# Kernel optimization log

Measured on AMD Instinct MI355X. Metric: run time of the kernel, lower is better.

The kernel has to match this reference:

```python
import jax, jax.numpy as jnp
import numpy as np

B, N_L, N_T, H, G = 8, 48, 512, 128, 10
BN_EPS = 1e-5


def setup_inputs() -> dict:
    key = jax.random.key(0)
    ks = jax.random.split(key, 16)
    inp = {
        "lig_s": jax.random.normal(ks[0], (B * N_L, H), dtype=jnp.float32),
        "lig_pos": jax.random.normal(ks[1], (B * N_L, 3), dtype=jnp.float32) * 5.0,
        "lig_batch": jnp.repeat(jnp.arange(B, dtype=jnp.int64), N_L),
        "pro_s": jax.random.normal(ks[2], (B * N_T, H), dtype=jnp.float32),
        "pro_pos": jax.random.normal(ks[3], (B * N_T, 3), dtype=jnp.float32) * 20.0,
        "pro_batch": jnp.repeat(jnp.arange(B, dtype=jnp.int64), N_T),
        # MLP: Linear(H,H) + BatchNorm1d(H) (eval mode) + ELU (+ Dropout off in eval)
        "W1": jax.random.normal(ks[4], (H, H), dtype=jnp.float32) / np.sqrt(H),
        "b1": jax.random.normal(ks[5], (H,), dtype=jnp.float32) * 0.01,
        "bn_gamma": 1.0 + 0.1 * jax.random.normal(ks[6], (H,), dtype=jnp.float32),
        "bn_beta": 0.1 * jax.random.normal(ks[7], (H,), dtype=jnp.float32),
        "bn_mean": 0.1 * jax.random.normal(ks[8], (H,), dtype=jnp.float32),
        "bn_var": 0.5 + jax.random.uniform(ks[9], (H,), dtype=jnp.float32),
        "W_pi": jax.random.normal(ks[10], (G, H), dtype=jnp.float32) / np.sqrt(H),
        "b_pi": jnp.zeros((G,), dtype=jnp.float32),
        "W_sigma": jax.random.normal(ks[11], (G, H), dtype=jnp.float32) / np.sqrt(H),
        "b_sigma": jnp.zeros((G,), dtype=jnp.float32),
        "W_mu": jax.random.normal(ks[12], (G, H), dtype=jnp.float32) / np.sqrt(H),
        "b_mu": jnp.zeros((G,), dtype=jnp.float32),
    }
    return inp


def _forward(lig_s, lig_pos, pro_s, pro_pos,
             W1, b1, bn_gamma, bn_beta, bn_mean, bn_var,
             W_pi, b_pi, W_sigma, b_sigma, W_mu, b_mu):
    # to_dense_batch with uniform graph sizes == reshape; C_mask is all-True,
    # so C[C_mask] == reshape(B*N_l*N_t, H).
    h_l = lig_s.reshape(B, N_L, H)
    h_t = pro_s.reshape(B, N_T, H)
    # broadcast pairwise sum: [B, N_l, N_t, H] -> compact to [M, H]
    C = (h_l[:, :, None, :] + h_t[:, None, :, :]).reshape(B * N_L * N_T, H)
    # MLP (eval mode): Linear -> BatchNorm1d(running stats) -> ELU
    C = C @ W1.T + b1
    C = (C - bn_mean) * jax.lax.rsqrt(bn_var + BN_EPS) * bn_gamma + bn_beta
    C = jax.nn.elu(C)
    pi = jax.nn.softmax(C @ W_pi.T + b_pi, axis=-1)
    sigma = jax.nn.elu(C @ W_sigma.T + b_sigma) + 1.1
    mu = jax.nn.elu(C @ W_mu.T + b_mu) + 1.0
    # pairwise Euclidean distances via -2*X@Y^T + |Y|^2 + |X|^2 (torch uses fp64;
    # fp32 here), then sqrt; compacted and detached.
    Xl = lig_pos.reshape(B, N_L, 3)
    Xt = pro_pos.reshape(B, N_T, 3)
    d2 = (-2.0 * jnp.einsum("bld,btd->blt", Xl, Xt)
          + jnp.sum(Xt * Xt, axis=-1)[:, None, :]
          + jnp.sum(Xl * Xl, axis=-1)[:, :, None])
    dist = jnp.sqrt(d2).reshape(B * N_L * N_T)
    dist = jax.lax.stop_gradient(dist[:, None])  # [M, 1]
    C_batch = jnp.repeat(jnp.arange(B, dtype=jnp.int64), N_L * N_T)
    return pi, sigma, mu, dist, C_batch


def reference(lig_s, lig_pos, lig_batch, pro_s, pro_pos, pro_batch,
              W1, b1, bn_gamma, bn_beta, bn_mean, bn_var,
              W_pi, b_pi, W_sigma, b_sigma, W_mu, b_mu):
    del lig_batch, pro_batch  # uniform segments -> reshape handles densification
    return _forward(lig_s, lig_pos, pro_s, pro_pos,
                    W1, b1, bn_gamma, bn_beta, bn_mean, bn_var,
                    W_pi, b_pi, W_sigma, b_sigma, W_mu, b_mu)
```

## Files before the change

### kernel.cpp

```cpp
#include <hip/hip_runtime.h>
#include <math.h>

constexpr int kB  = 8;
constexpr int kNL = 48;
constexpr int kNT = 512;
constexpr int kH  = 128;
constexpr int kG  = 10;

constexpr int kRowsL = kB * kNL;
constexpr int kRowsT = kB * kNT;
constexpr int kRows  = kRowsL + kRowsT;
constexpr int kM     = kB * kNL * kNT;
constexpr float kEps = 1e-5f;

constexpr size_t OFF_PI = 0;
constexpr size_t OFF_SG = (size_t)kM * kG;
constexpr size_t OFF_MU = 2 * (size_t)kM * kG;
constexpr size_t OFF_D  = 3 * (size_t)kM * kG;
constexpr size_t OFF_CB = OFF_D + kM;

typedef __attribute__((ext_vector_type(8))) short short8;
typedef __attribute__((ext_vector_type(4))) float f32x4;

__device__ __forceinline__ short f2bf(float f) {
    unsigned u = __builtin_bit_cast(unsigned, f);
    unsigned r = u + 0x7fffu + ((u >> 16) & 1u);
    return (short)(r >> 16);
}
__device__ __forceinline__ float elu_f(float x) {
    return x > 0.0f ? x : (__expf(x) - 1.0f);
}

__global__ __launch_bounds__(256) void pack_kernel(
    const float* __restrict__ W1, const float* __restrict__ b1,
    const float* __restrict__ gamma, const float* __restrict__ beta,
    const float* __restrict__ mean, const float* __restrict__ var,
    const float* __restrict__ Wpi, const float* __restrict__ Wsg,
    const float* __restrict__ Wmu,
    short* __restrict__ W1p, short* __restrict__ Wcp, float* __restrict__ bias_l)
{
    const int tid = threadIdx.x;
    __shared__ float s_s[kH];
    if (tid < kH) {
        float s = gamma[tid] * rsqrtf(var[tid] + kEps);
        s_s[tid] = s;
        bias_l[tid] = (b1[tid] - mean[tid]) * s + beta[tid];
    }
    __syncthreads();

    for (int idx = tid; idx < 4 * 8 * 64; idx += 256) {
        const int kt = idx >> 9, nt = (idx >> 6) & 7, lane = idx & 63;
        const int c  = nt * 16 + (lane & 15);
        const int k0 = kt * 32 + (lane >> 4) * 8;
        const float s = s_s[c];
        const float* wr = W1 + (size_t)c * kH + k0;
        short8 v;
#pragma unroll
        for (int j = 0; j < 8; ++j) v[j] = f2bf(wr[j] * s);
        *((short8*)W1p + idx) = v;
    }
    for (int idx = tid; idx < 4 * 3 * 64; idx += 256) {
        const int kt = idx / 192, rem = idx % 192, nt = rem >> 6, lane = rem & 63;
        const int n  = lane & 15;
        const int k0 = kt * 32 + (lane >> 4) * 8;
        const float* W = (nt == 0) ? Wpi : ((nt == 1) ? Wsg : Wmu);
        short8 v;
        if (n < kG) {
            const float* wr = W + (size_t)n * kH + k0;
#pragma unroll
            for (int j = 0; j < 8; ++j) v[j] = f2bf(wr[j]);
        } else {
#pragma unroll
            for (int j = 0; j < 8; ++j) v[j] = 0;
        }
        *((short8*)Wcp + idx) = v;
    }
}

__global__ __launch_bounds__(256) void prep_mfma(
    const float* __restrict__ lig_s, const float* __restrict__ pro_s,
    const short* __restrict__ W1p, const float* __restrict__ bias_l,
    float* __restrict__ Al, float* __restrict__ At)
{
    const int mtile = blockIdx.x;
    const int wave = threadIdx.x >> 6, lane = threadIdx.x & 63;
    const int q = lane >> 4, n16 = lane & 15;

    short8 bfrag[2][4];
    const short8* wp = (const short8*)W1p;
#pragma unroll
    for (int kt = 0; kt < 4; ++kt)
#pragma unroll
        for (int h = 0; h < 2; ++h)
            bfrag[h][kt] = wp[(kt * 8 + (2 * wave + h)) * 64 + lane];

    const int row = mtile * 16 + n16;
    const bool lig = (row < kRowsL);
    const float* X = lig ? (lig_s + (size_t)row * kH)
                         : (pro_s + (size_t)(row - kRowsL) * kH);

    f32x4 acc[2] = {};
#pragma unroll
    for (int kt = 0; kt < 4; ++kt) {
        const float4* xp = (const float4*)(X + kt * 32 + q * 8);
        float4 x0 = xp[0], x1 = xp[1];
        short8 a;
        a[0] = f2bf(x0.x); a[1] = f2bf(x0.y); a[2] = f2bf(x0.z); a[3] = f2bf(x0.w);
        a[4] = f2bf(x1.x); a[5] = f2bf(x1.y); a[6] = f2bf(x1.z); a[7] = f2bf(x1.w);
        acc[0] = __builtin_amdgcn_mfma_f32_16x16x32_bf16(a, bfrag[0][kt], acc[0], 0, 0, 0);
        acc[1] = __builtin_amdgcn_mfma_f32_16x16x32_bf16(a, bfrag[1][kt], acc[1], 0, 0, 0);
    }

#pragma unroll
    for (int h = 0; h < 2; ++h) {
        const int c = (2 * wave + h) * 16 + n16;
        const float bi = lig ? bias_l[c] : 0.0f;
#pragma unroll
        for (int r = 0; r < 4; ++r) {
            const int R = mtile * 16 + q * 4 + r;
            const float v = acc[h][r] + bi;
            if (lig) Al[(size_t)R * kH + c] = v;
            else     At[(size_t)(R - kRowsL) * kH + c] = v;
        }
    }
}

__global__ __launch_bounds__(256) void pair_mfma(
    const float* __restrict__ Al, const float* __restrict__ At,
    const short* __restrict__ Wcp,
    const float* __restrict__ bpi, const float* __restrict__ bsg,
    const float* __restrict__ bmu,
    float* __restrict__ out)
{
    const int blk = blockIdx.x;
    const int bl = blk >> 2, tch = blk & 3;
    const int wave = threadIdx.x >> 6, lane = threadIdx.x & 63;
    const int q = lane >> 4, n = lane & 15;
    const int b = bl / kNL;
    const int t0 = tch * 128 + wave * 32;

    short8 bf[3][4];
    const short8* wp = (const short8*)Wcp;
#pragma unroll
    for (int kt = 0; kt < 4; ++kt)
#pragma unroll
        for (int ntl = 0; ntl < 3; ++ntl)
            bf[ntl][kt] = wp[(kt * 3 + ntl) * 64 + lane];

    const int nc = (n < kG) ? n : (kG - 1);
    const float bias0 = (n < kG) ? bpi[nc] : 0.0f;
    const float bias1 = (n < kG) ? bsg[nc] : 0.0f;
    const float bias2 = (n < kG) ? bmu[nc] : 0.0f;

    const float* alp = Al + (size_t)bl * kH;
    f32x4 acc[2][3] = {};

#pragma unroll
    for (int mt = 0; mt < 2; ++mt) {
        const int t = t0 + mt * 16 + n;
        const float* atp = At + (size_t)(b * kNT + t) * kH;
#pragma unroll
        for (int kt = 0; kt < 4; ++kt) {
            const float4* ap4 = (const float4*)(alp + kt * 32 + q * 8);
            const float4* tp4 = (const float4*)(atp + kt * 32 + q * 8);
            float4 a0 = ap4[0], a1 = ap4[1];
            float4 t0v = tp4[0], t1v = tp4[1];
            short8 a;
            a[0] = f2bf(elu_f(a0.x + t0v.x)); a[1] = f2bf(elu_f(a0.y + t0v.y));
            a[2] = f2bf(elu_f(a0.z + t0v.z)); a[3] = f2bf(elu_f(a0.w + t0v.w));
            a[4] = f2bf(elu_f(a1.x + t1v.x)); a[5] = f2bf(elu_f(a1.y + t1v.y));
            a[6] = f2bf(elu_f(a1.z + t1v.z)); a[7] = f2bf(elu_f(a1.w + t1v.w));
            acc[mt][0] = __builtin_amdgcn_mfma_f32_16x16x32_bf16(a, bf[0][kt], acc[mt][0], 0, 0, 0);
            acc[mt][1] = __builtin_amdgcn_mfma_f32_16x16x32_bf16(a, bf[1][kt], acc[mt][1], 0, 0, 0);
            acc[mt][2] = __builtin_amdgcn_mfma_f32_16x16x32_bf16(a, bf[2][kt], acc[mt][2], 0, 0, 0);
        }
    }

    const int pairbase = bl * kNT + t0;
#pragma unroll
    for (int mt = 0; mt < 2; ++mt) {
#pragma unroll
        for (int r = 0; r < 4; ++r) {
            const float lg = acc[mt][0][r] + bias0;
            float mx = (n < kG) ? lg : -3.0e38f;
#pragma unroll
            for (int d = 1; d < 16; d <<= 1) mx = fmaxf(mx, __shfl_xor(mx, d));
            const float e = (n < kG) ? __expf(lg - mx) : 0.0f;
            float sm = e;
#pragma unroll
            for (int d = 1; d < 16; d <<= 1) sm += __shfl_xor(sm, d);
            const int m = pairbase + mt * 16 + q * 4 + r;
            if (n < kG) out[OFF_PI + (size_t)m * kG + n] = e / sm;
        }
#pragma unroll
        for (int r = 0; r < 4; ++r) {
            const int m = pairbase + mt * 16 + q * 4 + r;
            if (n < kG) {
                out[OFF_SG + (size_t)m * kG + n] = elu_f(acc[mt][1][r] + bias1) + 1.1f;
                out[OFF_MU + (size_t)m * kG + n] = elu_f(acc[mt][2][r] + bias2) + 1.0f;
            }
        }
    }
}

__global__ __launch_bounds__(256) void dist_kernel(
    const float* __restrict__ lig_pos, const float* __restrict__ pro_pos,
    float* __restrict__ out)
{
    const int idx = blockIdx.x * 256 + threadIdx.x;
    const int bl = idx >> 9, t = idx & 511;
    const int b = bl / kNL;
    const int pr = b * kNT + t;
    const float dx = lig_pos[(size_t)bl * 3 + 0] - pro_pos[(size_t)pr * 3 + 0];
    const float dy = lig_pos[(size_t)bl * 3 + 1] - pro_pos[(size_t)pr * 3 + 1];
    const float dz = lig_pos[(size_t)bl * 3 + 2] - pro_pos[(size_t)pr * 3 + 2];
    out[OFF_D + idx] = sqrtf(dx * dx + dy * dy + dz * dz);
    out[OFF_CB + idx] = (float)b;
}

extern "C" void kernel_launch(void* const* d_in, const int* in_sizes, int n_in,
                              void* d_out, int out_size, void* d_ws, size_t ws_size,
                              hipStream_t stream) {
    (void)in_sizes; (void)n_in; (void)out_size; (void)ws_size;
    const float* lig_s    = (const float*)d_in[0];
    const float* lig_pos  = (const float*)d_in[1];
    const float* pro_s    = (const float*)d_in[3];
    const float* pro_pos  = (const float*)d_in[4];
    const float* W1       = (const float*)d_in[6];
    const float* b1       = (const float*)d_in[7];
    const float* bn_gamma = (const float*)d_in[8];
    const float* bn_beta  = (const float*)d_in[9];
    const float* bn_mean  = (const float*)d_in[10];
    const float* bn_var   = (const float*)d_in[11];
    const float* W_pi     = (const float*)d_in[12];
    const float* b_pi     = (const float*)d_in[13];
    const float* W_sigma  = (const float*)d_in[14];
    const float* b_sigma  = (const float*)d_in[15];
    const float* W_mu     = (const float*)d_in[16];
    const float* b_mu     = (const float*)d_in[17];

    float* out = (float*)d_out;
    float* Al  = (float*)d_ws;
    float* At  = Al + (size_t)kRowsL * kH;
    short* W1p = (short*)(At + (size_t)kRowsT * kH);
    short* Wcp = W1p + 4 * 8 * 64 * 8;
    float* bias_l = (float*)(Wcp + 4 * 3 * 64 * 8);

    pack_kernel<<<1, 256, 0, stream>>>(W1, b1, bn_gamma, bn_beta, bn_mean, bn_var,
                                       W_pi, W_sigma, W_mu, W1p, Wcp, bias_l);
    prep_mfma<<<kRows / 16, 256, 0, stream>>>(lig_s, pro_s, W1p, bias_l, Al, At);
    pair_mfma<<<kRowsL * 4, 256, 0, stream>>>(Al, At, Wcp, b_pi, b_sigma, b_mu, out);
    dist_kernel<<<kM / 256, 256, 0, stream>>>(lig_pos, pro_pos, out);
}
```

Baseline: 128.8 us.

## Fuse weight packing into GEMM kernels, merge distance kernel, stage outputs via LDS

Drops the single-block pack kernel by having each block convert and BN-fold the weights into bf16 fragments directly from global memory. The distance and batch-index kernel is folded into the pair kernel, so four launches become two. Head outputs are staged in shared memory and written contiguously so global stores coalesce, and the ligand row is loaded once per block instead of once per tile. In exchange every block repeats the small weight conversion work.

```diff
diff --git a/kernel.cpp b/kernel.cpp
--- a/kernel.cpp
+++ b/kernel.cpp
@@ -31,71 +31,40 @@
     return x > 0.0f ? x : (__expf(x) - 1.0f);
 }
 
-__global__ __launch_bounds__(256) void pack_kernel(
+__global__ __launch_bounds__(256) void prep_fused(
+    const float* __restrict__ lig_s, const float* __restrict__ pro_s,
     const float* __restrict__ W1, const float* __restrict__ b1,
     const float* __restrict__ gamma, const float* __restrict__ beta,
     const float* __restrict__ mean, const float* __restrict__ var,
-    const float* __restrict__ Wpi, const float* __restrict__ Wsg,
-    const float* __restrict__ Wmu,
-    short* __restrict__ W1p, short* __restrict__ Wcp, float* __restrict__ bias_l)
-{
-    const int tid = threadIdx.x;
-    __shared__ float s_s[kH];
-    if (tid < kH) {
-        float s = gamma[tid] * rsqrtf(var[tid] + kEps);
-        s_s[tid] = s;
-        bias_l[tid] = (b1[tid] - mean[tid]) * s + beta[tid];
-    }
-    __syncthreads();
-
-    for (int idx = tid; idx < 4 * 8 * 64; idx += 256) {
-        const int kt = idx >> 9, nt = (idx >> 6) & 7, lane = idx & 63;
-        const int c  = nt * 16 + (lane & 15);
-        const int k0 = kt * 32 + (lane >> 4) * 8;
-        const float s = s_s[c];
-        const float* wr = W1 + (size_t)c * kH + k0;
-        short8 v;
-#pragma unroll
-        for (int j = 0; j < 8; ++j) v[j] = f2bf(wr[j] * s);
-        *((short8*)W1p + idx) = v;
-    }
-    for (int idx = tid; idx < 4 * 3 * 64; idx += 256) {
-        const int kt = idx / 192, rem = idx % 192, nt = rem >> 6, lane = rem & 63;
-        const int n  = lane & 15;
-        const int k0 = kt * 32 + (lane >> 4) * 8;
-        const float* W = (nt == 0) ? Wpi : ((nt == 1) ? Wsg : Wmu);
-        short8 v;
-        if (n < kG) {
-            const float* wr = W + (size_t)n * kH + k0;
-#pragma unroll
-            for (int j = 0; j < 8; ++j) v[j] = f2bf(wr[j]);
-        } else {
-#pragma unroll
-            for (int j = 0; j < 8; ++j) v[j] = 0;
-        }
-        *((short8*)Wcp + idx) = v;
-    }
-}
-
-__global__ __launch_bounds__(256) void prep_mfma(
-    const float* __restrict__ lig_s, const float* __restrict__ pro_s,
-    const short* __restrict__ W1p, const float* __restrict__ bias_l,
     float* __restrict__ Al, float* __restrict__ At)
 {
     const int mtile = blockIdx.x;
     const int wave = threadIdx.x >> 6, lane = threadIdx.x & 63;
     const int q = lane >> 4, n16 = lane & 15;
+    const bool lig = (mtile < kRowsL / 16);
 
     short8 bfrag[2][4];
-    const short8* wp = (const short8*)W1p;
-#pragma unroll
-    for (int kt = 0; kt < 4; ++kt)
-#pragma unroll
-        for (int h = 0; h < 2; ++h)
-            bfrag[h][kt] = wp[(kt * 8 + (2 * wave + h)) * 64 + lane];
+    float bi[2];
+#pragma unroll
+    for (int h = 0; h < 2; ++h) {
+        const int c = (2 * wave + h) * 16 + n16;
+        const float sc = gamma[c] * rsqrtf(var[c] + kEps);
+        bi[h] = lig ? ((b1[c] - mean[c]) * sc + beta[c]) : 0.0f;
+        const float* wr = W1 + (size_t)c * kH;
+#pragma unroll
+        for (int kt = 0; kt < 4; ++kt) {
+            const float4* w4 = (const float4*)(wr + kt * 32 + q * 8);
+            float4 w0 = w4[0], w1 = w4[1];
+            short8 v;
+            v[0] = f2bf(w0.x * sc); v[1] = f2bf(w0.y * sc);
+            v[2] = f2bf(w0.z * sc); v[3] = f2bf(w0.w * sc);
+            v[4] = f2bf(w1.x * sc); v[5] = f2bf(w1.y * sc);
+            v[6] = f2bf(w1.z * sc); v[7] = f2bf(w1.w * sc);
+            bfrag[h][kt] = v;
+        }
+    }
 
     const int row = mtile * 16 + n16;
-    const bool lig = (row < kRowsL);
     const float* X = lig ? (lig_s + (size_t)row * kH)
                          : (pro_s + (size_t)(row - kRowsL) * kH);
 
@@ -114,22 +83,22 @@
 #pragma unroll
     for (int h = 0; h < 2; ++h) {
         const int c = (2 * wave + h) * 16 + n16;
-        const float bi = lig ? bias_l[c] : 0.0f;
 #pragma unroll
         for (int r = 0; r < 4; ++r) {
             const int R = mtile * 16 + q * 4 + r;
-            const float v = acc[h][r] + bi;
+            const float v = acc[h][r] + bi[h];
             if (lig) Al[(size_t)R * kH + c] = v;
             else     At[(size_t)(R - kRowsL) * kH + c] = v;
         }
     }
 }
 
-__global__ __launch_bounds__(256) void pair_mfma(
+__global__ __launch_bounds__(256) void pair_fused(
     const float* __restrict__ Al, const float* __restrict__ At,
-    const short* __restrict__ Wcp,
-    const float* __restrict__ bpi, const float* __restrict__ bsg,
-    const float* __restrict__ bmu,
+    const float* __restrict__ Wpi, const float* __restrict__ bpi,
+    const float* __restrict__ Wsg, const float* __restrict__ bsg,
+    const float* __restrict__ Wmu, const float* __restrict__ bmu,
+    const float* __restrict__ lig_pos, const float* __restrict__ pro_pos,
     float* __restrict__ out)
 {
     const int blk = blockIdx.x;
@@ -140,31 +109,46 @@
     const int t0 = tch * 128 + wave * 32;
 
     short8 bf[3][4];
-    const short8* wp = (const short8*)Wcp;
-#pragma unroll
-    for (int kt = 0; kt < 4; ++kt)
-#pragma unroll
-        for (int ntl = 0; ntl < 3; ++ntl)
-            bf[ntl][kt] = wp[(kt * 3 + ntl) * 64 + lane];
-
-    const int nc = (n < kG) ? n : (kG - 1);
-    const float bias0 = (n < kG) ? bpi[nc] : 0.0f;
-    const float bias1 = (n < kG) ? bsg[nc] : 0.0f;
-    const float bias2 = (n < kG) ? bmu[nc] : 0.0f;
+#pragma unroll
+    for (int ntl = 0; ntl < 3; ++ntl) {
+        const float* W = (ntl == 0) ? Wpi : ((ntl == 1) ? Wsg : Wmu);
+#pragma unroll
+        for (int kt = 0; kt < 4; ++kt) {
+            short8 v;
+            if (n < kG) {
+                const float4* w4 = (const float4*)(W + (size_t)n * kH + kt * 32 + q * 8);
+                float4 w0 = w4[0], w1 = w4[1];
+                v[0] = f2bf(w0.x); v[1] = f2bf(w0.y); v[2] = f2bf(w0.z); v[3] = f2bf(w0.w);
+                v[4] = f2bf(w1.x); v[5] = f2bf(w1.y); v[6] = f2bf(w1.z); v[7] = f2bf(w1.w);
+            } else {
+#pragma unroll
+                for (int j = 0; j < 8; ++j) v[j] = 0;
+            }
+            bf[ntl][kt] = v;
+        }
+    }
+    const float bias0 = (n < kG) ? bpi[n] : 0.0f;
+    const float bias1 = (n < kG) ? bsg[n] : 0.0f;
+    const float bias2 = (n < kG) ? bmu[n] : 0.0f;
 
     const float* alp = Al + (size_t)bl * kH;
+    float4 al[4][2];
+#pragma unroll
+    for (int kt = 0; kt < 4; ++kt) {
+        const float4* ap4 = (const float4*)(alp + kt * 32 + q * 8);
+        al[kt][0] = ap4[0]; al[kt][1] = ap4[1];
+    }
+
     f32x4 acc[2][3] = {};
-
 #pragma unroll
     for (int mt = 0; mt < 2; ++mt) {
         const int t = t0 + mt * 16 + n;
         const float* atp = At + (size_t)(b * kNT + t) * kH;
 #pragma unroll
         for (int kt = 0; kt < 4; ++kt) {
-            const float4* ap4 = (const float4*)(alp + kt * 32 + q * 8);
             const float4* tp4 = (const float4*)(atp + kt * 32 + q * 8);
-            float4 a0 = ap4[0], a1 = ap4[1];
             float4 t0v = tp4[0], t1v = tp4[1];
+            const float4 a0 = al[kt][0], a1 = al[kt][1];
             short8 a;
             a[0] = f2bf(elu_f(a0.x + t0v.x)); a[1] = f2bf(elu_f(a0.y + t0v.y));
             a[2] = f2bf(elu_f(a0.z + t0v.z)); a[3] = f2bf(elu_f(a0.w + t0v.w));
@@ -176,11 +160,14 @@
         }
     }
 
-    const int pairbase = bl * kNT + t0;
+    __shared__ float st[4][3 * 320];
+    float* sw = st[wave];
+
 #pragma unroll
     for (int mt = 0; mt < 2; ++mt) {
 #pragma unroll
         for (int r = 0; r < 4; ++r) {
+            const int sl = (mt * 16 + q * 4 + r) * kG;
             const float lg = acc[mt][0][r] + bias0;
             float mx = (n < kG) ? lg : -3.0e38f;
 #pragma unroll
@@ -189,33 +176,36 @@
             float sm = e;
 #pragma unroll
             for (int d = 1; d < 16; d <<= 1) sm += __shfl_xor(sm, d);
-            const int m = pairbase + mt * 16 + q * 4 + r;
-            if (n < kG) out[OFF_PI + (size_t)m * kG + n] = e / sm;
-        }
-#pragma unroll
-        for (int r = 0; r < 4; ++r) {
-            const int m = pairbase + mt * 16 + q * 4 + r;
             if (n < kG) {
-                out[OFF_SG + (size_t)m * kG + n] = elu_f(acc[mt][1][r] + bias1) + 1.1f;
-                out[OFF_MU + (size_t)m * kG + n] = elu_f(acc[mt][2][r] + bias2) + 1.0f;
+                sw[sl + n]           = e / sm;
+                sw[320 + sl + n]     = elu_f(acc[mt][1][r] + bias1) + 1.1f;
+                sw[640 + sl + n]     = elu_f(acc[mt][2][r] + bias2) + 1.0f;
             }
         }
     }
-}
-
-__global__ __launch_bounds__(256) void dist_kernel(
-    const float* __restrict__ lig_pos, const float* __restrict__ pro_pos,
-    float* __restrict__ out)
-{
-    const int idx = blockIdx.x * 256 + threadIdx.x;
-    const int bl = idx >> 9, t = idx & 511;
-    const int b = bl / kNL;
-    const int pr = b * kNT + t;
-    const float dx = lig_pos[(size_t)bl * 3 + 0] - pro_pos[(size_t)pr * 3 + 0];
-    const float dy = lig_pos[(size_t)bl * 3 + 1] - pro_pos[(size_t)pr * 3 + 1];
-    const float dz = lig_pos[(size_t)bl * 3 + 2] - pro_pos[(size_t)pr * 3 + 2];
-    out[OFF_D + idx] = sqrtf(dx * dx + dy * dy + dz * dz);
-    out[OFF_CB + idx] = (float)b;
+    __syncthreads();
+
+    const int pairbase = bl * kNT + t0;
+    float* pib = out + OFF_PI + (size_t)pairbase * kG;
+    float* sgb = out + OFF_SG + (size_t)pairbase * kG;
+    float* mub = out + OFF_MU + (size_t)pairbase * kG;
+#pragma unroll
+    for (int i = 0; i < 5; ++i) {
+        pib[i * 64 + lane] = sw[i * 64 + lane];
+        sgb[i * 64 + lane] = sw[320 + i * 64 + lane];
+        mub[i * 64 + lane] = sw[640 + i * 64 + lane];
+    }
+
+    if (lane < 32) {
+        const int t = t0 + lane;
+        const int pr = b * kNT + t;
+        const int m = bl * kNT + t;
+        const float dx = lig_pos[(size_t)bl * 3 + 0] - pro_pos[(size_t)pr * 3 + 0];
+        const float dy = lig_pos[(size_t)bl * 3 + 1] - pro_pos[(size_t)pr * 3 + 1];
+        const float dz = lig_pos[(size_t)bl * 3 + 2] - pro_pos[(size_t)pr * 3 + 2];
+        out[OFF_D + m] = sqrtf(dx * dx + dy * dy + dz * dz);
+        out[OFF_CB + m] = (float)b;
+    }
 }
 
 extern "C" void kernel_launch(void* const* d_in, const int* in_sizes, int n_in,
@@ -242,13 +232,10 @@
     float* out = (float*)d_out;
     float* Al  = (float*)d_ws;
     float* At  = Al + (size_t)kRowsL * kH;
-    short* W1p = (short*)(At + (size_t)kRowsT * kH);
-    short* Wcp = W1p + 4 * 8 * 64 * 8;
-    float* bias_l = (float*)(Wcp + 4 * 3 * 64 * 8);
-
-    pack_kernel<<<1, 256, 0, stream>>>(W1, b1, bn_gamma, bn_beta, bn_mean, bn_var,
-                                       W_pi, W_sigma, W_mu, W1p, Wcp, bias_l);
-    prep_mfma<<<kRows / 16, 256, 0, stream>>>(lig_s, pro_s, W1p, bias_l, Al, At);
-    pair_mfma<<<kRowsL * 4, 256, 0, stream>>>(Al, At, Wcp, b_pi, b_sigma, b_mu, out);
-    dist_kernel<<<kM / 256, 256, 0, stream>>>(lig_pos, pro_pos, out);
-}
+
+    prep_fused<<<kRows / 16, 256, 0, stream>>>(
+        lig_s, pro_s, W1, b1, bn_gamma, bn_beta, bn_mean, bn_var, Al, At);
+    pair_fused<<<kRowsL * 4, 256, 0, stream>>>(
+        Al, At, W_pi, b_pi, W_sigma, b_sigma, W_mu, b_mu,
+        lig_pos, pro_pos, out);
+}
```

After: 134.0 us. +4.1%, slower.
